# Kernel optimization log

Measured on AMD Instinct MI355X. Metric: run time of the kernel, lower is better.

The kernel has to match this reference:

```python
import jax, jax.numpy as jnp
import numpy as np

NUM_HEADS = 16
HEAD_DIM = 128
HIDDEN = NUM_HEADS * HEAD_DIM


def rotate_half(x):
    x1, x2 = jnp.split(x, 2, axis=-1)
    return jnp.concatenate((-x2, x1), axis=-1)


def setup_inputs() -> dict:
    key = jax.random.key(0)
    ks = jax.random.split(key, 7)
    b, s = 2, 2048
    return {
        "hidden_states": jax.random.normal(ks[0], (b, s, HIDDEN), dtype=jnp.float32),
        "cos": jax.random.normal(ks[1], (1, 1, s, HEAD_DIM), dtype=jnp.float32),
        "sin": jax.random.normal(ks[2], (1, 1, s, HEAD_DIM), dtype=jnp.float32),
        "Wq": jax.random.normal(ks[3], (HIDDEN, HIDDEN), dtype=jnp.float32) * 0.02,
        "Wk": jax.random.normal(ks[4], (HIDDEN, HIDDEN), dtype=jnp.float32) * 0.02,
        "Wv": jax.random.normal(ks[5], (HIDDEN, HIDDEN), dtype=jnp.float32) * 0.02,
        "Wo": jax.random.normal(ks[6], (HIDDEN, HIDDEN), dtype=jnp.float32) * 0.02,
    }


def reference(hidden_states, cos, sin, Wq, Wk, Wv, Wo):
    b, s, _ = hidden_states.shape

    def proj(W):
        # [b,s,hidden] -> [b,H,s,D]
        return (hidden_states @ W).reshape(b, s, NUM_HEADS, HEAD_DIM).transpose(0, 2, 1, 3)

    q = proj(Wq)
    k = proj(Wk)
    v = proj(Wv)

    # RoPE: cos/sin [1,1,s,D] broadcast over batch and heads
    q = q * cos + rotate_half(q) * sin
    k = k * cos + rotate_half(k) * sin

    scale = 1.0 / jnp.sqrt(jnp.asarray(HEAD_DIM, dtype=q.dtype))
    scores = jnp.einsum("bhqd,bhkd->bhqk", q, k) * scale  # [b,H,s,s]
    attn = jax.nn.softmax(scores, axis=-1)  # no mask applied (matches source)
    out = jnp.einsum("bhqk,bhkd->bhqd", attn, v)  # [b,H,s,D]
    out = out.transpose(0, 2, 1, 3).reshape(b, s, HIDDEN)
    return out @ Wo
```

## Files before the change

### kernel.cpp

```cpp
#include <hip/hip_runtime.h>

typedef short bf16x8 __attribute__((ext_vector_type(8)));
typedef float f32x4 __attribute__((ext_vector_type(4)));

#define HID   2048
#define S_LEN 2048
#define NH    16
#define HD    128
#define BATCH 2
#define NROWS (BATCH * S_LEN)

__device__ __forceinline__ float bf2f(unsigned short u) {
    union { unsigned int i; float f; } v;
    v.i = ((unsigned int)u) << 16;
    return v.f;
}
__device__ __forceinline__ unsigned short f2bf(float f) {
    union { float f; unsigned int i; } v;
    v.f = f;
    unsigned int u = v.i;
    return (unsigned short)((u + 0x7fffu + ((u >> 16) & 1u)) >> 16);
}

__device__ __forceinline__ unsigned int pkbf(float a, float b) {
#if defined(__has_builtin) && __has_builtin(__builtin_amdgcn_cvt_pk_bf16_f32)
    typedef __bf16 bf2_t __attribute__((ext_vector_type(2)));
    bf2_t v = __builtin_amdgcn_cvt_pk_bf16_f32(a, b);
    unsigned int u;
    __builtin_memcpy(&u, &v, 4);
    return u;
#else
    return (unsigned int)f2bf(a) | ((unsigned int)f2bf(b) << 16);
#endif
}

__device__ __forceinline__ float exp2_fast(float x) {
#if defined(__has_builtin) && __has_builtin(__builtin_amdgcn_exp2f)
    return __builtin_amdgcn_exp2f(x);
#else
    return __expf(x * 0.6931471805599453f);
#endif
}

__device__ __forceinline__ void async16(const unsigned short* g, unsigned short* l) {
    __builtin_amdgcn_global_load_lds(
        (const __attribute__((address_space(1))) unsigned int*)g,
        (__attribute__((address_space(3))) unsigned int*)l, 16, 0, 0);
}

__global__ __launch_bounds__(256) void prep(const float* __restrict__ hs,
                                            const float* __restrict__ Wa,
                                            const float* __restrict__ Wb,
                                            const float* __restrict__ Wc,
                                            unsigned short* __restrict__ Xb,
                                            unsigned short* __restrict__ WT) {
    int z = blockIdx.z;
    int t = threadIdx.x;
    if (z == 3) {
        size_t idx = (((size_t)blockIdx.y * 64 + blockIdx.x) * 256 + t) * 8;
        float4 v0 = *(const float4*)(hs + idx);
        float4 v1 = *(const float4*)(hs + idx + 4);
        uint4 o;
        o.x = pkbf(v0.x, v0.y);
        o.y = pkbf(v0.z, v0.w);
        o.z = pkbf(v1.x, v1.y);
        o.w = pkbf(v1.z, v1.w);
        *(uint4*)(Xb + idx) = o;
        return;
    }
    __shared__ float tile[32][33];
    int tx = t & 31, ty = t >> 5;
    int bx = blockIdx.x, by = blockIdx.y;
    const float* W = (z == 0) ? Wa : ((z == 1) ? Wb : Wc);
    unsigned short* dst = WT + (size_t)z * HID * HID;
#pragma unroll
    for (int i = 0; i < 4; i++)
        tile[ty + i * 8][tx] = W[(size_t)(by * 32 + ty + i * 8) * HID + bx * 32 + tx];
    __syncthreads();
#pragma unroll
    for (int i = 0; i < 4; i++)
        dst[(size_t)(bx * 32 + ty + i * 8) * HID + by * 32 + tx] = f2bf(tile[tx][ty + i * 8]);
}

__global__ __launch_bounds__(256) void transpose_cast(const float* __restrict__ W,
                                                      unsigned short* __restrict__ WT) {
    __shared__ float tile[32][33];
    int t = threadIdx.x;
    int tx = t & 31, ty = t >> 5;
    int bx = blockIdx.x, by = blockIdx.y;
#pragma unroll
    for (int i = 0; i < 4; i++)
        tile[ty + i * 8][tx] = W[(size_t)(by * 32 + ty + i * 8) * HID + bx * 32 + tx];
    __syncthreads();
#pragma unroll
    for (int i = 0; i < 4; i++)
        WT[(size_t)(bx * 32 + ty + i * 8) * HID + by * 32 + tx] = f2bf(tile[tx][ty + i * 8]);
}

__global__ __launch_bounds__(512, 2) void gemm256(const unsigned short* __restrict__ A,
                                                  const unsigned short* __restrict__ Bt,
                                                  unsigned short* __restrict__ Qo,
                                                  unsigned short* __restrict__ Ko,
                                                  unsigned short* __restrict__ Vo,
                                                  const float* __restrict__ cosp,
                                                  const float* __restrict__ sinp) {
    __shared__ unsigned short SM[65536];
    int t = threadIdx.x;
    int wave = t >> 6, lane = t & 63;
    int wm = wave >> 2, wn = wave & 3;
    int c = lane & 15, quad = lane >> 4;
    int m0 = blockIdx.y * 256, n0 = blockIdx.x * 256;

    int lr = wave * 16 + (lane >> 2);
    int scw = ((lane & 3) ^ ((lane >> 2) & 3)) * 8;
    const unsigned short* Ag = A + (size_t)(m0 + lr) * HID + scw;
    const unsigned short* Bg = Bt + (size_t)(n0 + lr) * HID + scw;

    f32x4 zero = {0.f, 0.f, 0.f, 0.f};
    f32x4 acc[8][4];
#pragma unroll
    for (int i = 0; i < 8; i++)
#pragma unroll
        for (int j = 0; j < 4; j++) acc[i][j] = zero;

#pragma unroll
    for (int kt = 0; kt < 2; kt++) {
        unsigned short* Sl = SM + kt * 16384;
        async16(Ag + kt * 32, Sl + wave * 512);
        async16(Ag + kt * 32 + 128 * HID, Sl + wave * 512 + 4096);
        async16(Bg + kt * 32, Sl + 8192 + wave * 512);
        async16(Bg + kt * 32 + 128 * HID, Sl + 8192 + wave * 512 + 4096);
    }
    __builtin_amdgcn_s_waitcnt(0x0F74);
    __builtin_amdgcn_s_barrier();

    int cxor = (quad ^ (c & 3)) * 8;

#pragma unroll 4
    for (int kt = 0; kt < 64; kt++) {
        const unsigned short* Sa = SM + (kt & 3) * 16384;
        const unsigned short* Sb = Sa + 8192;
        int ktn = (kt + 2 > 63) ? 63 : kt + 2;
        unsigned short* Sn = SM + (ktn & 3) * 16384;

        async16(Ag + ktn * 32, Sn + wave * 512);
        async16(Ag + ktn * 32 + 128 * HID, Sn + wave * 512 + 4096);
        bf16x8 af[4], bfr[4];
#pragma unroll
        for (int mt = 0; mt < 4; mt++)
            af[mt] = *(const bf16x8*)(Sa + (wm * 128 + mt * 16 + c) * 32 + cxor);
#pragma unroll
        for (int nt = 0; nt < 4; nt++)
            bfr[nt] = *(const bf16x8*)(Sb + (wn * 64 + nt * 16 + c) * 32 + cxor);
        __builtin_amdgcn_s_barrier();
        __builtin_amdgcn_s_setprio(1);
#pragma unroll
        for (int mt = 0; mt < 4; mt++)
#pragma unroll
            for (int nt = 0; nt < 4; nt++)
                acc[mt][nt] = __builtin_amdgcn_mfma_f32_16x16x32_bf16(af[mt], bfr[nt],
                                                                      acc[mt][nt], 0, 0, 0);
        __builtin_amdgcn_s_setprio(0);
        __builtin_amdgcn_s_barrier();

        async16(Bg + ktn * 32, Sn + 8192 + wave * 512);
        async16(Bg + ktn * 32 + 128 * HID, Sn + 8192 + wave * 512 + 4096);
#pragma unroll
        for (int mt = 0; mt < 4; mt++)
            af[mt] = *(const bf16x8*)(Sa + (wm * 128 + (mt + 4) * 16 + c) * 32 + cxor);
        __builtin_amdgcn_s_waitcnt(0x0F74);
        __builtin_amdgcn_s_barrier();
        __builtin_amdgcn_s_setprio(1);
#pragma unroll
        for (int mt = 0; mt < 4; mt++)
#pragma unroll
            for (int nt = 0; nt < 4; nt++)
                acc[mt + 4][nt] = __builtin_amdgcn_mfma_f32_16x16x32_bf16(af[mt], bfr[nt],
                                                                          acc[mt + 4][nt], 0, 0, 0);
        __builtin_amdgcn_s_setprio(0);
        __builtin_amdgcn_s_barrier();
    }

    __syncthreads();

    int mat = n0 >> 11;
    int hbase = (n0 & 2047) >> 7;
    int h = hbase + (wn >> 1);
    if (mat == 2) {
#pragma unroll
        for (int mt = 0; mt < 8; mt++)
#pragma unroll
            for (int nt = 0; nt < 4; nt++) {
                int d = (wn & 1) * 64 + nt * 16 + c;
                int row0 = m0 + wm * 128 + mt * 16 + quad * 4;
                int b = row0 >> 11, s = row0 & 2047;
                ushort4 o;
                o.x = f2bf(acc[mt][nt][0]);
                o.y = f2bf(acc[mt][nt][1]);
                o.z = f2bf(acc[mt][nt][2]);
                o.w = f2bf(acc[mt][nt][3]);
                *(ushort4*)(Vo + ((size_t)(b * NH + h) * HD + d) * S_LEN + s) = o;
            }
    } else {
        unsigned short* Cb = (mat == 0) ? Qo : Ko;
        float scl = (mat == 0) ? 0.12751743f : 1.0f;
#pragma unroll
        for (int mt = 0; mt < 8; mt++)
#pragma unroll
            for (int nt = 0; nt < 4; nt++) {
                ushort4 o;
                o.x = f2bf(acc[mt][nt][0]);
                o.y = f2bf(acc[mt][nt][1]);
                o.z = f2bf(acc[mt][nt][2]);
                o.w = f2bf(acc[mt][nt][3]);
                *(ushort4*)(SM + (mt * 4 + nt) * 2048 + t * 4) = o;
            }
        __syncthreads();
        int partner = (wave ^ 1) * 64 + lane;
        float sgn = (wn & 1) ? 1.0f : -1.0f;
#pragma unroll
        for (int mt = 0; mt < 8; mt++) {
#pragma unroll
            for (int nt = 0; nt < 4; nt++) {
                ushort4 pv = *(const ushort4*)(SM + (mt * 4 + nt) * 2048 + partner * 4);
                float part[4] = {bf2f(pv.x), bf2f(pv.y), bf2f(pv.z), bf2f(pv.w)};
                int d = (wn & 1) * 64 + nt * 16 + c;
#pragma unroll
                for (int r = 0; r < 4; r++) {
                    int row = m0 + wm * 128 + mt * 16 + quad * 4 + r;
                    int b = row >> 11, s = row & 2047;
                    float cv = cosp[s * HD + d], sv = sinp[s * HD + d];
                    float out = (acc[mt][nt][r] * cv + sgn * part[r] * sv) * scl;
                    Cb[((size_t)(b * NH + h) * S_LEN + s) * HD + d] = f2bf(out);
                }
            }
        }
    }
}

template <int MODE>
__global__ __launch_bounds__(256, 2) void gemm_bt(const unsigned short* __restrict__ A,
                                                  const unsigned short* __restrict__ Bt,
                                                  unsigned short* __restrict__ Qo,
                                                  unsigned short* __restrict__ Ko,
                                                  unsigned short* __restrict__ Vo,
                                                  float* __restrict__ Fo,
                                                  const float* __restrict__ cosp,
                                                  const float* __restrict__ sinp,
                                                  int n_shift) {
    __shared__ unsigned short SM[16384];
    unsigned short* Asm = SM;
    unsigned short* Bsm = SM + 8192;
    int t = threadIdx.x;
    int wave = t >> 6, lane = t & 63;
    int wm = wave >> 1, wn = wave & 1;
    int c = lane & 15, quad = lane >> 4;
    int m0 = blockIdx.y * 128, nloc = blockIdx.x * 128;

    int lr = lane >> 3;
    int cb = (lane & 7) ^ (lr & 7);
    const unsigned short* Ag = A + (size_t)(m0 + wave * 32 + lr) * HID + cb * 8;
    const unsigned short* Bg = Bt + (size_t)(nloc + wave * 32 + lr) * HID + cb * 8;
    unsigned short* Al = Asm + wave * 2048;
    unsigned short* Bl = Bsm + wave * 2048;

    f32x4 zero = {0.f, 0.f, 0.f, 0.f};
    f32x4 acc[4][4];
#pragma unroll
    for (int i = 0; i < 4; i++)
#pragma unroll
        for (int j = 0; j < 4; j++) acc[i][j] = zero;

    for (int it = 0; it < 32; it++) {
        int k0 = it * 64;
#pragma unroll
        for (int j = 0; j < 4; j++) {
            async16(Ag + k0 + j * 8 * HID, Al + j * 512);
            async16(Bg + k0 + j * 8 * HID, Bl + j * 512);
        }
        __syncthreads();
#pragma unroll
        for (int kk = 0; kk < 2; kk++) {
            bf16x8 af[4], bfr[4];
#pragma unroll
            for (int mt = 0; mt < 4; mt++)
                af[mt] = *(const bf16x8*)(Asm + (wm * 64 + mt * 16 + c) * 64 +
                                          (((kk * 4 + quad) ^ (c & 7)) * 8));
#pragma unroll
            for (int nt = 0; nt < 4; nt++)
                bfr[nt] = *(const bf16x8*)(Bsm + (wn * 64 + nt * 16 + c) * 64 +
                                           (((kk * 4 + quad) ^ (c & 7)) * 8));
#pragma unroll
            for (int mt = 0; mt < 4; mt++)
#pragma unroll
                for (int nt = 0; nt < 4; nt++)
                    acc[mt][nt] = __builtin_amdgcn_mfma_f32_16x16x32_bf16(af[mt], bfr[nt],
                                                                          acc[mt][nt], 0, 0, 0);
        }
        __syncthreads();
    }

    if (MODE == 2) {
#pragma unroll
        for (int mt = 0; mt < 4; mt++)
#pragma unroll
            for (int nt = 0; nt < 4; nt++)
#pragma unroll
                for (int r = 0; r < 4; r++) {
                    int row = m0 + wm * 64 + mt * 16 + quad * 4 + r;
                    int col = nloc + wn * 64 + nt * 16 + c;
                    Fo[(size_t)row * HID + col] = acc[mt][nt][r];
                }
    } else {
        int nglob0 = n_shift + nloc;
        int mat = nglob0 >> 11;
        int h = (nglob0 & 2047) >> 7;
        if (mat == 2) {
#pragma unroll
            for (int mt = 0; mt < 4; mt++)
#pragma unroll
                for (int nt = 0; nt < 4; nt++) {
                    int d = wn * 64 + nt * 16 + c;
                    int row0 = m0 + wm * 64 + mt * 16 + quad * 4;
                    int b = row0 >> 11, s = row0 & 2047;
                    ushort4 o;
                    o.x = f2bf(acc[mt][nt][0]);
                    o.y = f2bf(acc[mt][nt][1]);
                    o.z = f2bf(acc[mt][nt][2]);
                    o.w = f2bf(acc[mt][nt][3]);
                    *(ushort4*)(Vo + ((size_t)(b * NH + h) * HD + d) * S_LEN + s) = o;
                }
        } else {
            unsigned short* Cb = (mat == 0) ? Qo : Ko;
            float scl = (mat == 0) ? 0.12751743f : 1.0f;
            __syncthreads();
#pragma unroll
            for (int mt = 0; mt < 4; mt++)
#pragma unroll
                for (int nt = 0; nt < 4; nt++) {
                    ushort4 o;
                    o.x = f2bf(acc[mt][nt][0]);
                    o.y = f2bf(acc[mt][nt][1]);
                    o.z = f2bf(acc[mt][nt][2]);
                    o.w = f2bf(acc[mt][nt][3]);
                    *(ushort4*)(SM + (mt * 4 + nt) * 1024 + t * 4) = o;
                }
            __syncthreads();
            int partner = (wm * 2 + (wn ^ 1)) * 64 + lane;
            float sgn = wn ? 1.0f : -1.0f;
#pragma unroll
            for (int mt = 0; mt < 4; mt++) {
#pragma unroll
                for (int nt = 0; nt < 4; nt++) {
                    ushort4 pv = *(const ushort4*)(SM + (mt * 4 + nt) * 1024 + partner * 4);
                    float part[4] = {bf2f(pv.x), bf2f(pv.y), bf2f(pv.z), bf2f(pv.w)};
                    int col = wn * 64 + nt * 16 + c;
#pragma unroll
                    for (int r = 0; r < 4; r++) {
                        int row = m0 + wm * 64 + mt * 16 + quad * 4 + r;
                        int b = row >> 11, s = row & 2047;
                        float cv = cosp[s * HD + col], sv = sinp[s * HD + col];
                        float out = (acc[mt][nt][r] * cv + sgn * part[r] * sv) * scl;
                        Cb[((size_t)(b * NH + h) * S_LEN + s) * HD + col] = f2bf(out);
                    }
                }
            }
        }
    }
}

#define PKS 72
__global__ __launch_bounds__(256, 2) void attn_kernel(const unsigned short* __restrict__ Q,
                                                      const unsigned short* __restrict__ Kg,
                                                      const unsigned short* __restrict__ Vt,
                                                      unsigned short* __restrict__ Aout) {
    __shared__ unsigned short Ksm[64 * 128];
    __shared__ unsigned short Vsm[128 * 64];
    __shared__ __align__(16) unsigned short Psm[4 * 2 * 16 * PKS];
    int bh = blockIdx.y;
    int b = bh >> 4, h = bh & 15;
    int t = threadIdx.x;
    int wave = t >> 6, lane = t & 63;
    int c = lane & 15, quad = lane >> 4;
    int q0 = blockIdx.x * 128 + wave * 32;
    const unsigned short* Qp = Q + (size_t)bh * S_LEN * HD;
    const unsigned short* Kp = Kg + (size_t)bh * S_LEN * HD;
    const unsigned short* Vp = Vt + (size_t)bh * HD * S_LEN;

    bf16x8 qf[2][4];
#pragma unroll
    for (int qn = 0; qn < 2; qn++)
#pragma unroll
        for (int kk = 0; kk < 4; kk++)
            qf[qn][kk] = *(const bf16x8*)(Qp + (size_t)(q0 + qn * 16 + c) * HD + kk * 32 + quad * 8);

    f32x4 zero = {0.f, 0.f, 0.f, 0.f};
    f32x4 o_acc[2][8];
#pragma unroll
    for (int qn = 0; qn < 2; qn++)
#pragma unroll
        for (int nt = 0; nt < 8; nt++) o_acc[qn][nt] = zero;
    float lsum[2] = {0.f, 0.f};

    for (int key0 = 0; key0 < S_LEN; key0 += 64) {
#pragma unroll
        for (int j = 0; j < 4; j++) {
            int fc = (wave * 4 + j) * 64 + lane;
            int rK = fc >> 4, cbK = (fc & 15) ^ (rK & 15);
            async16(Kp + (size_t)(key0 + rK) * HD + cbK * 8, Ksm + (wave * 4 + j) * 512);
            int rV = fc >> 3, cbV = (fc & 7) ^ (rV & 7);
            async16(Vp + (size_t)rV * S_LEN + key0 + cbV * 8, Vsm + (wave * 4 + j) * 512);
        }
        __syncthreads();

        f32x4 sacc[4][2];
#pragma unroll
        for (int km = 0; km < 4; km++)
#pragma unroll
            for (int qn = 0; qn < 2; qn++) sacc[km][qn] = zero;
#pragma unroll
        for (int kk = 0; kk < 4; kk++) {
            bf16x8 kfr[4];
#pragma unroll
            for (int km = 0; km < 4; km++)
                kfr[km] = *(const bf16x8*)(Ksm + (km * 16 + c) * HD + (((kk * 4 + quad) ^ c)) * 8);
#pragma unroll
            for (int km = 0; km < 4; km++)
#pragma unroll
                for (int qn = 0; qn < 2; qn++)
                    sacc[km][qn] = __builtin_amdgcn_mfma_f32_16x16x32_bf16(kfr[km], qf[qn][kk],
                                                                           sacc[km][qn], 0, 0, 0);
        }

#pragma unroll
        for (int qn = 0; qn < 2; qn++) {
#pragma unroll
            for (int km = 0; km < 4; km++) {
                float e0 = exp2_fast(sacc[km][qn][0]);
                float e1 = exp2_fast(sacc[km][qn][1]);
                float e2 = exp2_fast(sacc[km][qn][2]);
                float e3 = exp2_fast(sacc[km][qn][3]);
                lsum[qn] += (e0 + e1) + (e2 + e3);
                uint2 pk;
                pk.x = pkbf(e0, e1);
                pk.y = pkbf(e2, e3);
                *(uint2*)(Psm + ((wave * 2 + qn) * 16 + c) * PKS + km * 16 + quad * 4) = pk;
            }
        }
        asm volatile("" ::: "memory");
        __builtin_amdgcn_s_waitcnt(0xc07f);
        asm volatile("" ::: "memory");

#pragma unroll
        for (int kf = 0; kf < 2; kf++) {
            bf16x8 pf[2];
#pragma unroll
            for (int qn = 0; qn < 2; qn++)
                pf[qn] = *(const bf16x8*)(Psm + ((wave * 2 + qn) * 16 + c) * PKS + kf * 32 + quad * 8);
#pragma unroll
            for (int nt = 0; nt < 8; nt++) {
                bf16x8 vf = *(const bf16x8*)(Vsm + (nt * 16 + c) * 64 +
                                             (((kf * 4 + quad) ^ (c & 7))) * 8);
#pragma unroll
                for (int qn = 0; qn < 2; qn++)
                    o_acc[qn][nt] = __builtin_amdgcn_mfma_f32_16x16x32_bf16(pf[qn], vf,
                                                                            o_acc[qn][nt], 0, 0, 0);
            }
        }
        __syncthreads();
    }

#pragma unroll
    for (int qn = 0; qn < 2; qn++) {
        lsum[qn] += __shfl_xor(lsum[qn], 16);
        lsum[qn] += __shfl_xor(lsum[qn], 32);
    }
    float inv[2][4];
#pragma unroll
    for (int qn = 0; qn < 2; qn++)
#pragma unroll
        for (int r = 0; r < 4; r++)
            inv[qn][r] = 1.0f / __shfl(lsum[qn], quad * 4 + r);

#pragma unroll
    for (int qn = 0; qn < 2; qn++) {
#pragma unroll
        for (int r = 0; r < 4; r++) {
            int srow = q0 + qn * 16 + quad * 4 + r;
            size_t base = ((size_t)(b * S_LEN + srow)) * HID + h * HD;
#pragma unroll
            for (int nt = 0; nt < 8; nt++)
                Aout[base + nt * 16 + c] = f2bf(o_acc[qn][nt][r] * inv[qn][r]);
        }
    }
}

extern "C" void kernel_launch(void* const* d_in, const int* in_sizes, int n_in,
                              void* d_out, int out_size, void* d_ws, size_t ws_size,
                              hipStream_t stream) {
    const float* hs   = (const float*)d_in[0];
    const float* cosp = (const float*)d_in[1];
    const float* sinp = (const float*)d_in[2];
    const float* Wq   = (const float*)d_in[3];
    const float* Wk   = (const float*)d_in[4];
    const float* Wv   = (const float*)d_in[5];
    const float* Wo   = (const float*)d_in[6];

    char* ws = (char*)d_ws;
    unsigned short* Xb = (unsigned short*)(ws);
    unsigned short* Qb = (unsigned short*)(ws + (16ull << 20));
    unsigned short* Kb = (unsigned short*)(ws + (32ull << 20));
    unsigned short* Vb = (unsigned short*)(ws + (48ull << 20));
    unsigned short* WT = (unsigned short*)(ws + (64ull << 20));

    const bool fused = ws_size >= (88ull << 20);

    if (fused) {
        prep<<<dim3(64, 64, 4), 256, 0, stream>>>(hs, Wq, Wk, Wv, Xb, WT);
        gemm256<<<dim3(24, 16), 512, 0, stream>>>(Xb, WT, Qb, Kb, Vb, cosp, sinp);
        attn_kernel<<<dim3(16, 32), 256, 0, stream>>>(Qb, Kb, Vb, Xb );
        unsigned short* WoT = (unsigned short*)(ws + (16ull << 20));
        transpose_cast<<<dim3(64, 64), 256, 0, stream>>>(Wo, WoT);
        gemm_bt<2><<<dim3(16, 32), 256, 0, stream>>>(Xb, WoT, nullptr, nullptr, nullptr,
                                                     (float*)d_out, cosp, sinp, 0);
    } else {
        prep<<<dim3(64, 64, 1), 256, 0, stream>>>(hs, Wq, Wq, Wq, Xb, WT);
        prep<<<dim3(64, 64, 4), 256, 0, stream>>>(hs, Wq, Wq, Wq, Xb, WT);
        gemm_bt<0><<<dim3(16, 32), 256, 0, stream>>>(Xb, WT, Qb, Kb, Vb, nullptr,
                                                     cosp, sinp, 0);
        transpose_cast<<<dim3(64, 64), 256, 0, stream>>>(Wk, WT);
        gemm_bt<0><<<dim3(16, 32), 256, 0, stream>>>(Xb, WT, Qb, Kb, Vb, nullptr,
                                                     cosp, sinp, 2048);
        transpose_cast<<<dim3(64, 64), 256, 0, stream>>>(Wv, WT);
        gemm_bt<0><<<dim3(16, 32), 256, 0, stream>>>(Xb, WT, Qb, Kb, Vb, nullptr,
                                                     cosp, sinp, 4096);
        attn_kernel<<<dim3(16, 32), 256, 0, stream>>>(Qb, Kb, Vb, Xb );
        transpose_cast<<<dim3(64, 64), 256, 0, stream>>>(Wo, WT);
        gemm_bt<2><<<dim3(16, 32), 256, 0, stream>>>(Xb, WT, nullptr, nullptr, nullptr,
                                                     (float*)d_out, cosp, sinp, 0);
    }
}
```

Before: 451.6 us.

## Retile fused QKV GEMM to 128x384 tiles with triple-buffered LDS and swizzled block order

```diff
diff --git a/kernel.cpp b/kernel.cpp
--- a/kernel.cpp
+++ b/kernel.cpp
@@ -97,144 +97,147 @@
         WT[(size_t)(bx * 32 + ty + i * 8) * HID + by * 32 + tx] = f2bf(tile[tx][ty + i * 8]);
 }
 
-__global__ __launch_bounds__(512, 2) void gemm256(const unsigned short* __restrict__ A,
-                                                  const unsigned short* __restrict__ Bt,
-                                                  unsigned short* __restrict__ Qo,
-                                                  unsigned short* __restrict__ Ko,
-                                                  unsigned short* __restrict__ Vo,
-                                                  const float* __restrict__ cosp,
-                                                  const float* __restrict__ sinp) {
-    __shared__ unsigned short SM[65536];
+__global__ __launch_bounds__(512, 2) void gemm_qkv(const unsigned short* __restrict__ A,
+                                                   const unsigned short* __restrict__ Bt,
+                                                   unsigned short* __restrict__ Qo,
+                                                   unsigned short* __restrict__ Ko,
+                                                   unsigned short* __restrict__ Vo,
+                                                   const float* __restrict__ cosp,
+                                                   const float* __restrict__ sinp) {
+    __shared__ unsigned short SM[49152];
     int t = threadIdx.x;
-    int wave = t >> 6, lane = t & 63;
-    int wm = wave >> 2, wn = wave & 3;
+    int w = t >> 6, lane = t & 63;
+    int wm = w >> 2, wn = w & 3;
     int c = lane & 15, quad = lane >> 4;
-    int m0 = blockIdx.y * 256, n0 = blockIdx.x * 256;
-
-    int lr = wave * 16 + (lane >> 2);
-    int scw = ((lane & 3) ^ ((lane >> 2) & 3)) * 8;
-    const unsigned short* Ag = A + (size_t)(m0 + lr) * HID + scw;
-    const unsigned short* Bg = Bt + (size_t)(n0 + lr) * HID + scw;
+
+    int bid = blockIdx.x;
+    int wgid = (bid & 7) * 64 + (bid >> 3);
+    int bx = wgid >> 5, by = wgid & 31;
+    int m0 = by * 128, n0 = bx * 384;
+
+    int srow = lane >> 2;
+    int schk = (lane & 3) ^ ((lane >> 3) & 3);
+    const unsigned short* Agp = A  + (size_t)(m0 + w * 16 + srow) * HID + schk * 8;
+    const unsigned short* Bgp = Bt + (size_t)(n0 + w * 16 + srow) * HID + schk * 8;
 
     f32x4 zero = {0.f, 0.f, 0.f, 0.f};
-    f32x4 acc[8][4];
-#pragma unroll
-    for (int i = 0; i < 8; i++)
-#pragma unroll
-        for (int j = 0; j < 4; j++) acc[i][j] = zero;
-
-#pragma unroll
-    for (int kt = 0; kt < 2; kt++) {
-        unsigned short* Sl = SM + kt * 16384;
-        async16(Ag + kt * 32, Sl + wave * 512);
-        async16(Ag + kt * 32 + 128 * HID, Sl + wave * 512 + 4096);
-        async16(Bg + kt * 32, Sl + 8192 + wave * 512);
-        async16(Bg + kt * 32 + 128 * HID, Sl + 8192 + wave * 512 + 4096);
+    f32x4 acc[4][6];
+#pragma unroll
+    for (int i = 0; i < 4; i++)
+#pragma unroll
+        for (int j = 0; j < 6; j++) acc[i][j] = zero;
+
+#pragma unroll
+    for (int p = 0; p < 2; p++) {
+        unsigned short* S = SM + p * 16384;
+        async16(Agp + p * 32, S + w * 512);
+#pragma unroll
+        for (int j = 0; j < 3; j++)
+            async16(Bgp + p * 32 + (size_t)j * 128 * HID, S + 4096 + j * 4096 + w * 512);
     }
     __builtin_amdgcn_s_waitcnt(0x0F74);
     __builtin_amdgcn_s_barrier();
 
-    int cxor = (quad ^ (c & 3)) * 8;
-
-#pragma unroll 4
+    int rofs = (quad ^ ((c >> 1) & 3)) * 8;
+
+    int scur = 0;
     for (int kt = 0; kt < 64; kt++) {
-        const unsigned short* Sa = SM + (kt & 3) * 16384;
-        const unsigned short* Sb = Sa + 8192;
-        int ktn = (kt + 2 > 63) ? 63 : kt + 2;
-        unsigned short* Sn = SM + (ktn & 3) * 16384;
-
-        async16(Ag + ktn * 32, Sn + wave * 512);
-        async16(Ag + ktn * 32 + 128 * HID, Sn + wave * 512 + 4096);
-        bf16x8 af[4], bfr[4];
-#pragma unroll
-        for (int mt = 0; mt < 4; mt++)
-            af[mt] = *(const bf16x8*)(Sa + (wm * 128 + mt * 16 + c) * 32 + cxor);
-#pragma unroll
-        for (int nt = 0; nt < 4; nt++)
-            bfr[nt] = *(const bf16x8*)(Sb + (wn * 64 + nt * 16 + c) * 32 + cxor);
+        const unsigned short* Sa = SM + scur * 16384;
+        const unsigned short* Sb = Sa + 4096;
+        int ktn = kt + 2; if (ktn > 63) ktn = 63;
+        int snx = scur + 2; if (snx >= 3) snx -= 3;
+        unsigned short* Sn = SM + snx * 16384;
+
+        async16(Agp + ktn * 32, Sn + w * 512);
+        bf16x8 af[2], bfr[6];
+#pragma unroll
+        for (int mt = 0; mt < 2; mt++)
+            af[mt] = *(const bf16x8*)(Sa + (wm * 64 + mt * 16 + c) * 32 + rofs);
+#pragma unroll
+        for (int nt = 0; nt < 6; nt++)
+            bfr[nt] = *(const bf16x8*)(Sb + (wn * 96 + nt * 16 + c) * 32 + rofs);
         __builtin_amdgcn_s_barrier();
         __builtin_amdgcn_s_setprio(1);
 #pragma unroll
-        for (int mt = 0; mt < 4; mt++)
-#pragma unroll
-            for (int nt = 0; nt < 4; nt++)
+        for (int mt = 0; mt < 2; mt++)
+#pragma unroll
+            for (int nt = 0; nt < 6; nt++)
                 acc[mt][nt] = __builtin_amdgcn_mfma_f32_16x16x32_bf16(af[mt], bfr[nt],
                                                                       acc[mt][nt], 0, 0, 0);
         __builtin_amdgcn_s_setprio(0);
         __builtin_amdgcn_s_barrier();
 
-        async16(Bg + ktn * 32, Sn + 8192 + wave * 512);
-        async16(Bg + ktn * 32 + 128 * HID, Sn + 8192 + wave * 512 + 4096);
-#pragma unroll
-        for (int mt = 0; mt < 4; mt++)
-            af[mt] = *(const bf16x8*)(Sa + (wm * 128 + (mt + 4) * 16 + c) * 32 + cxor);
+#pragma unroll
+        for (int j = 0; j < 3; j++)
+            async16(Bgp + ktn * 32 + (size_t)j * 128 * HID, Sn + 4096 + j * 4096 + w * 512);
+        bf16x8 ag[2];
+#pragma unroll
+        for (int mt = 0; mt < 2; mt++)
+            ag[mt] = *(const bf16x8*)(Sa + (wm * 64 + (mt + 2) * 16 + c) * 32 + rofs);
         __builtin_amdgcn_s_waitcnt(0x0F74);
         __builtin_amdgcn_s_barrier();
         __builtin_amdgcn_s_setprio(1);
 #pragma unroll
-        for (int mt = 0; mt < 4; mt++)
-#pragma unroll
-            for (int nt = 0; nt < 4; nt++)
-                acc[mt + 4][nt] = __builtin_amdgcn_mfma_f32_16x16x32_bf16(af[mt], bfr[nt],
-                                                                          acc[mt + 4][nt], 0, 0, 0);
+        for (int mt = 0; mt < 2; mt++)
+#pragma unroll
+            for (int nt = 0; nt < 6; nt++)
+                acc[mt + 2][nt] = __builtin_amdgcn_mfma_f32_16x16x32_bf16(ag[mt], bfr[nt],
+                                                                          acc[mt + 2][nt], 0, 0, 0);
         __builtin_amdgcn_s_setprio(0);
         __builtin_amdgcn_s_barrier();
+
+        scur = (scur + 1 == 3) ? 0 : scur + 1;
     }
 
     __syncthreads();
 
-    int mat = n0 >> 11;
-    int hbase = (n0 & 2047) >> 7;
-    int h = hbase + (wn >> 1);
-    if (mat == 2) {
-#pragma unroll
-        for (int mt = 0; mt < 8; mt++)
-#pragma unroll
-            for (int nt = 0; nt < 4; nt++) {
-                int d = (wn & 1) * 64 + nt * 16 + c;
-                int row0 = m0 + wm * 128 + mt * 16 + quad * 4;
+#pragma unroll
+    for (int mt = 0; mt < 4; mt++) {
+#pragma unroll
+        for (int nt = 0; nt < 6; nt++) {
+            ushort4 o;
+            o.x = f2bf(acc[mt][nt][0]);
+            o.y = f2bf(acc[mt][nt][1]);
+            o.z = f2bf(acc[mt][nt][2]);
+            o.w = f2bf(acc[mt][nt][3]);
+            *(ushort4*)(SM + (w * 6 + nt) * 256 + lane * 4) = o;
+        }
+        __syncthreads();
+#pragma unroll
+        for (int nt = 0; nt < 6; nt++) {
+            int colbase = n0 + wn * 96 + nt * 16;
+            int mat = colbase >> 11;
+            int h = (colbase & 2047) >> 7;
+            int dc = (colbase & 127) + c;
+            if (mat == 2) {
+                int row0 = m0 + wm * 64 + mt * 16 + quad * 4;
                 int b = row0 >> 11, s = row0 & 2047;
                 ushort4 o;
                 o.x = f2bf(acc[mt][nt][0]);
                 o.y = f2bf(acc[mt][nt][1]);
                 o.z = f2bf(acc[mt][nt][2]);
                 o.w = f2bf(acc[mt][nt][3]);
-                *(ushort4*)(Vo + ((size_t)(b * NH + h) * HD + d) * S_LEN + s) = o;
-            }
-    } else {
-        unsigned short* Cb = (mat == 0) ? Qo : Ko;
-        float scl = (mat == 0) ? 0.12751743f : 1.0f;
-#pragma unroll
-        for (int mt = 0; mt < 8; mt++)
-#pragma unroll
-            for (int nt = 0; nt < 4; nt++) {
-                ushort4 o;
-                o.x = f2bf(acc[mt][nt][0]);
-                o.y = f2bf(acc[mt][nt][1]);
-                o.z = f2bf(acc[mt][nt][2]);
-                o.w = f2bf(acc[mt][nt][3]);
-                *(ushort4*)(SM + (mt * 4 + nt) * 2048 + t * 4) = o;
-            }
-        __syncthreads();
-        int partner = (wave ^ 1) * 64 + lane;
-        float sgn = (wn & 1) ? 1.0f : -1.0f;
-#pragma unroll
-        for (int mt = 0; mt < 8; mt++) {
-#pragma unroll
-            for (int nt = 0; nt < 4; nt++) {
-                ushort4 pv = *(const ushort4*)(SM + (mt * 4 + nt) * 2048 + partner * 4);
+                *(ushort4*)(Vo + ((size_t)(b * NH + h) * HD + dc) * S_LEN + s) = o;
+            } else {
+                int q2 = (wn * 96 + nt * 16) ^ 64;
+                int wn2 = q2 / 96;
+                int nt2 = (q2 - wn2 * 96) >> 4;
+                ushort4 pv = *(const ushort4*)(SM + ((wm * 4 + wn2) * 6 + nt2) * 256 + lane * 4);
                 float part[4] = {bf2f(pv.x), bf2f(pv.y), bf2f(pv.z), bf2f(pv.w)};
-                int d = (wn & 1) * 64 + nt * 16 + c;
+                float sgn = ((colbase >> 6) & 1) ? 1.0f : -1.0f;
+                unsigned short* Cb = (mat == 0) ? Qo : Ko;
+                float scl = (mat == 0) ? 0.12751743f : 1.0f;
 #pragma unroll
                 for (int r = 0; r < 4; r++) {
-                    int row = m0 + wm * 128 + mt * 16 + quad * 4 + r;
+                    int row = m0 + wm * 64 + mt * 16 + quad * 4 + r;
                     int b = row >> 11, s = row & 2047;
-                    float cv = cosp[s * HD + d], sv = sinp[s * HD + d];
+                    float cv = cosp[s * HD + dc], sv = sinp[s * HD + dc];
                     float out = (acc[mt][nt][r] * cv + sgn * part[r] * sv) * scl;
-                    Cb[((size_t)(b * NH + h) * S_LEN + s) * HD + d] = f2bf(out);
+                    Cb[((size_t)(b * NH + h) * S_LEN + s) * HD + dc] = f2bf(out);
                 }
             }
         }
+        __syncthreads();
     }
 }
 
@@ -517,7 +520,7 @@
 
     if (fused) {
         prep<<<dim3(64, 64, 4), 256, 0, stream>>>(hs, Wq, Wk, Wv, Xb, WT);
-        gemm256<<<dim3(24, 16), 512, 0, stream>>>(Xb, WT, Qb, Kb, Vb, cosp, sinp);
+        gemm_qkv<<<dim3(512), 512, 0, stream>>>(Xb, WT, Qb, Kb, Vb, cosp, sinp);
         attn_kernel<<<dim3(16, 32), 256, 0, stream>>>(Qb, Kb, Vb, Xb );
         unsigned short* WoT = (unsigned short*)(ws + (16ull << 20));
         transpose_cast<<<dim3(64, 64), 256, 0, stream>>>(Wo, WoT);
```

Result: faster. 395.6 us (-12.4%).

## Restructure QKV GEMM to K=64 double-buffered tiles with XCD-aware block remap

Applied to the files above, without the earlier changes.

```diff
diff --git a/kernel.cpp b/kernel.cpp
--- a/kernel.cpp
+++ b/kernel.cpp
@@ -97,24 +97,28 @@
         WT[(size_t)(bx * 32 + ty + i * 8) * HID + by * 32 + tx] = f2bf(tile[tx][ty + i * 8]);
 }
 
-__global__ __launch_bounds__(512, 2) void gemm256(const unsigned short* __restrict__ A,
-                                                  const unsigned short* __restrict__ Bt,
-                                                  unsigned short* __restrict__ Qo,
-                                                  unsigned short* __restrict__ Ko,
-                                                  unsigned short* __restrict__ Vo,
-                                                  const float* __restrict__ cosp,
-                                                  const float* __restrict__ sinp) {
+__global__ __launch_bounds__(512, 2) void gemm_qkv(const unsigned short* __restrict__ A,
+                                                   const unsigned short* __restrict__ Bt,
+                                                   unsigned short* __restrict__ Qo,
+                                                   unsigned short* __restrict__ Ko,
+                                                   unsigned short* __restrict__ Vo,
+                                                   const float* __restrict__ cosp,
+                                                   const float* __restrict__ sinp) {
     __shared__ unsigned short SM[65536];
     int t = threadIdx.x;
-    int wave = t >> 6, lane = t & 63;
-    int wm = wave >> 2, wn = wave & 3;
+    int w = t >> 6, lane = t & 63;
+    int wm = w >> 2, wn = w & 3;
     int c = lane & 15, quad = lane >> 4;
-    int m0 = blockIdx.y * 256, n0 = blockIdx.x * 256;
-
-    int lr = wave * 16 + (lane >> 2);
-    int scw = ((lane & 3) ^ ((lane >> 2) & 3)) * 8;
-    const unsigned short* Ag = A + (size_t)(m0 + lr) * HID + scw;
-    const unsigned short* Bg = Bt + (size_t)(n0 + lr) * HID + scw;
+
+    int bid = blockIdx.x;
+    int wgid = (bid & 7) * 48 + (bid >> 3);
+    int bx = wgid >> 4, by = wgid & 15;
+    int m0 = by * 256, n0 = bx * 256;
+
+    int lr = lane >> 3;
+    int cb = (lane & 7) ^ (lr & 7);
+    const unsigned short* Agp = A  + (size_t)(m0 + w * 8 + lr) * HID + cb * 8;
+    const unsigned short* Bgp = Bt + (size_t)(n0 + w * 8 + lr) * HID + cb * 8;
 
     f32x4 zero = {0.f, 0.f, 0.f, 0.f};
     f32x4 acc[8][4];
@@ -123,63 +127,116 @@
 #pragma unroll
         for (int j = 0; j < 4; j++) acc[i][j] = zero;
 
-#pragma unroll
-    for (int kt = 0; kt < 2; kt++) {
-        unsigned short* Sl = SM + kt * 16384;
-        async16(Ag + kt * 32, Sl + wave * 512);
-        async16(Ag + kt * 32 + 128 * HID, Sl + wave * 512 + 4096);
-        async16(Bg + kt * 32, Sl + 8192 + wave * 512);
-        async16(Bg + kt * 32 + 128 * HID, Sl + 8192 + wave * 512 + 4096);
-    }
-    __builtin_amdgcn_s_waitcnt(0x0F74);
+#define ST(BUF, MTX, J, KT) async16(                                            \
+        ((MTX) ? Bgp : Agp) + (KT) * 64 + (size_t)(J) * 64 * HID,               \
+        SM + (BUF) * 32768 + (MTX) * 16384 + (J) * 4096 + w * 512)
+
+    ST(0, 1, 0, 0); ST(0, 1, 1, 0); ST(0, 1, 2, 0); ST(0, 1, 3, 0);
+    ST(0, 0, 0, 0); ST(0, 0, 2, 0); ST(0, 0, 1, 0); ST(0, 0, 3, 0);
+    __builtin_amdgcn_s_waitcnt(0x0F70);
     __builtin_amdgcn_s_barrier();
 
-    int cxor = (quad ^ (c & 3)) * 8;
-
-#pragma unroll 4
-    for (int kt = 0; kt < 64; kt++) {
-        const unsigned short* Sa = SM + (kt & 3) * 16384;
-        const unsigned short* Sb = Sa + 8192;
-        int ktn = (kt + 2 > 63) ? 63 : kt + 2;
-        unsigned short* Sn = SM + (ktn & 3) * 16384;
-
-        async16(Ag + ktn * 32, Sn + wave * 512);
-        async16(Ag + ktn * 32 + 128 * HID, Sn + wave * 512 + 4096);
-        bf16x8 af[4], bfr[4];
-#pragma unroll
-        for (int mt = 0; mt < 4; mt++)
-            af[mt] = *(const bf16x8*)(Sa + (wm * 128 + mt * 16 + c) * 32 + cxor);
+#pragma unroll 1
+    for (int kt = 0; kt < 32; kt++) {
+        const unsigned short* Ab = SM + (kt & 1) * 32768;
+        const unsigned short* Bb = Ab + 16384;
+        int ktn = kt + 1; if (ktn > 31) ktn = 31;
+        int nb = (kt + 1) & 1;
+        bf16x8 bfr[4][2], af[2][2];
+
 #pragma unroll
         for (int nt = 0; nt < 4; nt++)
-            bfr[nt] = *(const bf16x8*)(Sb + (wn * 64 + nt * 16 + c) * 32 + cxor);
-        __builtin_amdgcn_s_barrier();
+#pragma unroll
+            for (int kk = 0; kk < 2; kk++)
+                bfr[nt][kk] = *(const bf16x8*)(Bb + (wn * 64 + nt * 16 + c) * 64 +
+                                               (((kk * 4 + quad) ^ (c & 7)) * 8));
+#pragma unroll
+        for (int mt = 0; mt < 2; mt++)
+#pragma unroll
+            for (int kk = 0; kk < 2; kk++)
+                af[mt][kk] = *(const bf16x8*)(Ab + (wm * 128 + mt * 16 + c) * 64 +
+                                              (((kk * 4 + quad) ^ (c & 7)) * 8));
+        ST(nb, 1, 0, ktn); ST(nb, 1, 1, ktn);
+        __builtin_amdgcn_s_barrier();
+        __builtin_amdgcn_sched_barrier(0);
         __builtin_amdgcn_s_setprio(1);
 #pragma unroll
-        for (int mt = 0; mt < 4; mt++)
+        for (int mt = 0; mt < 2; mt++)
 #pragma unroll
             for (int nt = 0; nt < 4; nt++)
-                acc[mt][nt] = __builtin_amdgcn_mfma_f32_16x16x32_bf16(af[mt], bfr[nt],
-                                                                      acc[mt][nt], 0, 0, 0);
+#pragma unroll
+                for (int kk = 0; kk < 2; kk++)
+                    acc[mt][nt] = __builtin_amdgcn_mfma_f32_16x16x32_bf16(
+                        af[mt][kk], bfr[nt][kk], acc[mt][nt], 0, 0, 0);
         __builtin_amdgcn_s_setprio(0);
         __builtin_amdgcn_s_barrier();
 
-        async16(Bg + ktn * 32, Sn + 8192 + wave * 512);
-        async16(Bg + ktn * 32 + 128 * HID, Sn + 8192 + wave * 512 + 4096);
-#pragma unroll
-        for (int mt = 0; mt < 4; mt++)
-            af[mt] = *(const bf16x8*)(Sa + (wm * 128 + (mt + 4) * 16 + c) * 32 + cxor);
+#pragma unroll
+        for (int mt = 0; mt < 2; mt++)
+#pragma unroll
+            for (int kk = 0; kk < 2; kk++)
+                af[mt][kk] = *(const bf16x8*)(Ab + (wm * 128 + (mt + 2) * 16 + c) * 64 +
+                                              (((kk * 4 + quad) ^ (c & 7)) * 8));
+        ST(nb, 1, 2, ktn); ST(nb, 1, 3, ktn);
         __builtin_amdgcn_s_waitcnt(0x0F74);
         __builtin_amdgcn_s_barrier();
+        __builtin_amdgcn_sched_barrier(0);
         __builtin_amdgcn_s_setprio(1);
 #pragma unroll
-        for (int mt = 0; mt < 4; mt++)
+        for (int mt = 0; mt < 2; mt++)
 #pragma unroll
             for (int nt = 0; nt < 4; nt++)
-                acc[mt + 4][nt] = __builtin_amdgcn_mfma_f32_16x16x32_bf16(af[mt], bfr[nt],
-                                                                          acc[mt + 4][nt], 0, 0, 0);
+#pragma unroll
+                for (int kk = 0; kk < 2; kk++)
+                    acc[mt + 2][nt] = __builtin_amdgcn_mfma_f32_16x16x32_bf16(
+                        af[mt][kk], bfr[nt][kk], acc[mt + 2][nt], 0, 0, 0);
         __builtin_amdgcn_s_setprio(0);
         __builtin_amdgcn_s_barrier();
-    }
+
+#pragma unroll
+        for (int mt = 0; mt < 2; mt++)
+#pragma unroll
+            for (int kk = 0; kk < 2; kk++)
+                af[mt][kk] = *(const bf16x8*)(Ab + (wm * 128 + (mt + 4) * 16 + c) * 64 +
+                                              (((kk * 4 + quad) ^ (c & 7)) * 8));
+        ST(nb, 0, 0, ktn); ST(nb, 0, 2, ktn);
+        __builtin_amdgcn_s_barrier();
+        __builtin_amdgcn_sched_barrier(0);
+        __builtin_amdgcn_s_setprio(1);
+#pragma unroll
+        for (int mt = 0; mt < 2; mt++)
+#pragma unroll
+            for (int nt = 0; nt < 4; nt++)
+#pragma unroll
+                for (int kk = 0; kk < 2; kk++)
+                    acc[mt + 4][nt] = __builtin_amdgcn_mfma_f32_16x16x32_bf16(
+                        af[mt][kk], bfr[nt][kk], acc[mt + 4][nt], 0, 0, 0);
+        __builtin_amdgcn_s_setprio(0);
+        __builtin_amdgcn_s_barrier();
+
+#pragma unroll
+        for (int mt = 0; mt < 2; mt++)
+#pragma unroll
+            for (int kk = 0; kk < 2; kk++)
+                af[mt][kk] = *(const bf16x8*)(Ab + (wm * 128 + (mt + 6) * 16 + c) * 64 +
+                                              (((kk * 4 + quad) ^ (c & 7)) * 8));
+        ST(nb, 0, 1, ktn); ST(nb, 0, 3, ktn);
+        __builtin_amdgcn_s_waitcnt(0x0F72);
+        __builtin_amdgcn_s_barrier();
+        __builtin_amdgcn_sched_barrier(0);
+        __builtin_amdgcn_s_setprio(1);
+#pragma unroll
+        for (int mt = 0; mt < 2; mt++)
+#pragma unroll
+            for (int nt = 0; nt < 4; nt++)
+#pragma unroll
+                for (int kk = 0; kk < 2; kk++)
+                    acc[mt + 6][nt] = __builtin_amdgcn_mfma_f32_16x16x32_bf16(
+                        af[mt][kk], bfr[nt][kk], acc[mt + 6][nt], 0, 0, 0);
+        __builtin_amdgcn_s_setprio(0);
+        __builtin_amdgcn_s_barrier();
+    }
+#undef ST
 
     __syncthreads();
 
@@ -216,7 +273,7 @@
                 *(ushort4*)(SM + (mt * 4 + nt) * 2048 + t * 4) = o;
             }
         __syncthreads();
-        int partner = (wave ^ 1) * 64 + lane;
+        int partner = (w ^ 1) * 64 + lane;
         float sgn = (wn & 1) ? 1.0f : -1.0f;
 #pragma unroll
         for (int mt = 0; mt < 8; mt++) {
@@ -517,7 +574,7 @@
 
     if (fused) {
         prep<<<dim3(64, 64, 4), 256, 0, stream>>>(hs, Wq, Wk, Wv, Xb, WT);
-        gemm256<<<dim3(24, 16), 512, 0, stream>>>(Xb, WT, Qb, Kb, Vb, cosp, sinp);
+        gemm_qkv<<<dim3(384), 512, 0, stream>>>(Xb, WT, Qb, Kb, Vb, cosp, sinp);
         attn_kernel<<<dim3(16, 32), 256, 0, stream>>>(Qb, Kb, Vb, Xb );
         unsigned short* WoT = (unsigned short*)(ws + (16ull << 20));
         transpose_cast<<<dim3(64, 64), 256, 0, stream>>>(Wo, WoT);
```

New measurement: 473.5 us. 1.05x slower.
